# Performance work log

Hardware: AMD Instinct MI355X
Metric: run time of the kernel (lower is better)

Reference implementation:

```python
import jax, jax.numpy as jnp
import numpy as np

EPS = 1e-12  # torch F.normalize eps


def _l2norm(x):
    n = jnp.sqrt(jnp.sum(x * x, axis=-1, keepdims=True))
    return x / jnp.maximum(n, EPS)


def setup_inputs() -> dict:
    key = jax.random.key(0)
    k1, k2, k3, k4 = jax.random.split(key, 4)
    Bq, Lq, Bd, Ld, H, D = 128, 32, 128, 128, 256, 128
    return {
        "query_h": jax.random.normal(k1, (Bq, Lq, H), dtype=jnp.float32),
        "doc_h": jax.random.normal(k2, (Bd, Ld, H), dtype=jnp.float32),
        "W": jax.random.normal(k3, (H, D), dtype=jnp.float32) * 0.02,
        "b": jax.random.normal(k4, (D,), dtype=jnp.float32) * 0.02,
    }


def reference(query_h, doc_h, W, b):
    # token_mapper + L2 normalize (as in embed())
    q = _l2norm(query_h @ W + b)          # [Bq, Lq, D]
    d = _l2norm(doc_h @ W + b)            # [Bd, Ld, D]
    # max_sim: cross-product bmm(doc, query^T) -> [Bq, Bd, Ld, Lq]
    scores = jnp.einsum('qsd,btd->qbts', q, d)
    # max over doc tokens (dim=1 of bmm output), sum over query tokens (dim=2)
    logits = jnp.sum(jnp.max(scores, axis=2), axis=2)  # [Bq, Bd]
    return logits
```

## Files before the change

kernel.cpp:

```cpp
#include <hip/hip_runtime.h>

typedef unsigned short u16;
typedef __attribute__((ext_vector_type(8))) short short8;
typedef __attribute__((ext_vector_type(16))) float f32x16;
typedef __attribute__((ext_vector_type(4))) float f32x4;
typedef __attribute__((ext_vector_type(2))) float f32x2;
typedef __attribute__((ext_vector_type(4))) unsigned int u32x4;

#define H 256
#define D 128


static __device__ inline u16 f32_to_bf16(float f) {
    unsigned u = __float_as_uint(f);
    unsigned r = u + 0x7FFFu + ((u >> 16) & 1u);
    return (u16)(r >> 16);
}

__global__ __launch_bounds__(256) void proj_norm_fused(
    const float* __restrict__ Xq, const float* __restrict__ Xd,
    const float* __restrict__ W,  const float* __restrict__ bias,
    u16* __restrict__ outq, u16* __restrict__ outd)
{
    __shared__ float xs[64][33];
    __shared__ float ws[64][128];
    const int blk = blockIdx.x;
    const float* X;
    u16* out;
    int tok0;
    if (blk < 128) { X = Xq; out = outq; tok0 = blk * 32; }
    else           { X = Xd; out = outd; tok0 = (blk - 128) * 32; }

    const int tid = threadIdx.x;
    const int tg = tid >> 5;
    const int dg = tid & 31;

    float acc[4][4] = {{0.f}};

    for (int h0 = 0; h0 < H; h0 += 64) {
        {
            int c  = tid & 15;
            int tp = tid >> 4;
            #pragma unroll
            for (int pass = 0; pass < 2; ++pass) {
                int t = tp + pass * 16;
                f32x4 v = *(const f32x4*)&X[(size_t)(tok0 + t) * H + h0 + c * 4];
                xs[c*4+0][t] = v.x;
                xs[c*4+1][t] = v.y;
                xs[c*4+2][t] = v.z;
                xs[c*4+3][t] = v.w;
            }
        }
        {
            int dcol = tid & 31;
            int hrow = tid >> 5;
            #pragma unroll
            for (int pass = 0; pass < 8; ++pass) {
                int hh = hrow + pass * 8;
                *(f32x4*)&ws[hh][dcol*4] =
                    *(const f32x4*)&W[(size_t)(h0 + hh) * D + dcol * 4];
            }
        }
        __syncthreads();
        #pragma unroll 8
        for (int hh = 0; hh < 64; ++hh) {
            float x0 = xs[hh][tg*4+0];
            float x1 = xs[hh][tg*4+1];
            float x2 = xs[hh][tg*4+2];
            float x3 = xs[hh][tg*4+3];
            f32x4 wv = *(const f32x4*)&ws[hh][dg*4];
            #pragma unroll
            for (int j = 0; j < 4; ++j) {
                acc[0][j] += x0 * wv[j];
                acc[1][j] += x1 * wv[j];
                acc[2][j] += x2 * wv[j];
                acc[3][j] += x3 * wv[j];
            }
        }
        __syncthreads();
    }

    f32x4 bv = *(const f32x4*)&bias[dg * 4];
    #pragma unroll
    for (int i = 0; i < 4; ++i)
        #pragma unroll
        for (int j = 0; j < 4; ++j)
            acc[i][j] += bv[j];

    const int kc   = dg >> 2;
    const int lg2  = (dg >> 1) & 1;
    const int par  = dg & 1;
    const size_t tileBase = (size_t)(tok0 >> 5) * 4096;

    #pragma unroll
    for (int i = 0; i < 4; ++i) {
        float ss = acc[i][0]*acc[i][0] + acc[i][1]*acc[i][1]
                 + acc[i][2]*acc[i][2] + acc[i][3]*acc[i][3];
        ss += __shfl_xor(ss, 1);
        ss += __shfl_xor(ss, 2);
        ss += __shfl_xor(ss, 4);
        ss += __shfl_xor(ss, 8);
        ss += __shfl_xor(ss, 16);
        float n   = sqrtf(ss);
        float inv = 1.0f / fmaxf(n, 1e-12f);
        unsigned p0 = (unsigned)f32_to_bf16(acc[i][0]*inv) |
                      ((unsigned)f32_to_bf16(acc[i][1]*inv) << 16);
        unsigned p1 = (unsigned)f32_to_bf16(acc[i][2]*inv) |
                      ((unsigned)f32_to_bf16(acc[i][3]*inv) << 16);
        unsigned q0 = __shfl_xor(p0, 1);
        unsigned q1 = __shfl_xor(p1, 1);
        if ((par == 0) == (i < 2)) {
            u32x4 ck;
            if (par == 0) { ck.x = p0; ck.y = p1; ck.z = q0; ck.w = q1; }
            else          { ck.x = q0; ck.y = q1; ck.z = p0; ck.w = p1; }
            int l31 = tg * 4 + i;
            *(u32x4*)&out[tileBase + kc * 512 + l31 * 16 + lg2 * 8] = ck;
        }
    }
}

__global__ __launch_bounds__(256) void maxsim_kernel(
    const u16* __restrict__ qbf, const u16* __restrict__ dbf,
    float* __restrict__ logits)
{
    __shared__ float smax[4][8][2][32];
    const int tid  = threadIdx.x;
    const int wid  = tid >> 6;
    const int lane = tid & 63;
    const int l31  = lane & 31;
    const int soff = ((lane & 31) * 2 + (lane >> 5)) * 8;

    const int qb0 = (blockIdx.x >> 4) * 2;
    const int db0 = (blockIdx.x & 15) * 8;

    short8 bq[2][8];
    #pragma unroll
    for (int qs = 0; qs < 2; ++qs) {
        const u16* qb_base = qbf + (size_t)(qb0 + qs) * 4096 + soff;
        #pragma unroll
        for (int kc = 0; kc < 8; ++kc)
            bq[qs][kc] = *(const short8*)(qb_base + kc * 512);
    }

    #pragma unroll 2
    for (int dbi = 0; dbi < 8; ++dbi) {
        const u16* dt = dbf + (size_t)((db0 + dbi) * 4 + wid) * 4096 + soff;
        short8 af[8];
        #pragma unroll
        for (int kc = 0; kc < 8; ++kc)
            af[kc] = *(const short8*)(dt + kc * 512);

        f32x16 acc0 = {0.f}, acc1 = {0.f};
        #pragma unroll
        for (int kc = 0; kc < 8; ++kc) {
            acc0 = __builtin_amdgcn_mfma_f32_32x32x16_bf16(af[kc], bq[0][kc], acc0, 0, 0, 0);
            acc1 = __builtin_amdgcn_mfma_f32_32x32x16_bf16(af[kc], bq[1][kc], acc1, 0, 0, 0);
        }

        #pragma unroll
        for (int qs = 0; qs < 2; ++qs) {
            const f32x16 a = qs ? acc1 : acc0;
            float m0 = fmaxf(a[0], a[1]),   m1 = fmaxf(a[2], a[3]);
            float m2 = fmaxf(a[4], a[5]),   m3 = fmaxf(a[6], a[7]);
            float m4 = fmaxf(a[8], a[9]),   m5 = fmaxf(a[10], a[11]);
            float m6 = fmaxf(a[12], a[13]), m7 = fmaxf(a[14], a[15]);
            float m = fmaxf(fmaxf(fmaxf(m0, m1), fmaxf(m2, m3)),
                            fmaxf(fmaxf(m4, m5), fmaxf(m6, m7)));
            m = fmaxf(m, __shfl_xor(m, 32));
            if (lane < 32) smax[wid][dbi][qs][l31] = m;
        }
    }
    __syncthreads();

    {
        const int dbi = tid >> 5;
        const int col = tid & 31;
        float v0 = fmaxf(fmaxf(smax[0][dbi][0][col], smax[1][dbi][0][col]),
                         fmaxf(smax[2][dbi][0][col], smax[3][dbi][0][col]));
        float v1 = fmaxf(fmaxf(smax[0][dbi][1][col], smax[1][dbi][1][col]),
                         fmaxf(smax[2][dbi][1][col], smax[3][dbi][1][col]));
        v0 += __shfl_xor(v0, 1);  v1 += __shfl_xor(v1, 1);
        v0 += __shfl_xor(v0, 2);  v1 += __shfl_xor(v1, 2);
        v0 += __shfl_xor(v0, 4);  v1 += __shfl_xor(v1, 4);
        v0 += __shfl_xor(v0, 8);  v1 += __shfl_xor(v1, 8);
        v0 += __shfl_xor(v0, 16); v1 += __shfl_xor(v1, 16);
        if (col == 0) {
            logits[(size_t)qb0 * 128 + db0 + dbi]       = v0;
            logits[(size_t)(qb0 + 1) * 128 + db0 + dbi] = v1;
        }
    }
}

extern "C" void kernel_launch(void* const* d_in, const int* in_sizes, int n_in,
                              void* d_out, int out_size, void* d_ws, size_t ws_size,
                              hipStream_t stream)
{
    const float* query_h = (const float*)d_in[0];
    const float* doc_h   = (const float*)d_in[1];
    const float* W       = (const float*)d_in[2];
    const float* bias    = (const float*)d_in[3];
    float* logits = (float*)d_out;

    u16* qbf = (u16*)d_ws;
    u16* dbf = qbf + (size_t)128 * 4096;

    proj_norm_fused<<<dim3(640), dim3(256), 0, stream>>>(query_h, doc_h, W, bias, qbf, dbf);
    maxsim_kernel<<<dim3(1024), dim3(256), 0, stream>>>(qbf, dbf, logits);
}
```

Measured before the change: 114.5 us.

## Replace FP32 FMA projection with split-bf16 MFMA projection and W pre-pack

The scalar FP32 shared-memory GEMM for the token projection is replaced by MFMA 32x32x16 bf16 instructions. Each operand is split into a high bf16 part and a low residual, and three MFMAs per tile approximate FP32 accuracy. A new small prep kernel packs W into hi/lo bf16 fragments laid out for the MFMA. Normalization and the tiled bf16 output layout are recomputed from the MFMA accumulator layout. This adds a kernel launch and leaves only 160 blocks, which may underfill the GPU.

```diff
diff --git a/kernel.cpp b/kernel.cpp
--- a/kernel.cpp
+++ b/kernel.cpp
@@ -1,120 +1,149 @@
 #include <hip/hip_runtime.h>
 
 typedef unsigned short u16;
+typedef unsigned int u32;
 typedef __attribute__((ext_vector_type(8))) short short8;
 typedef __attribute__((ext_vector_type(16))) float f32x16;
 typedef __attribute__((ext_vector_type(4))) float f32x4;
-typedef __attribute__((ext_vector_type(2))) float f32x2;
 typedef __attribute__((ext_vector_type(4))) unsigned int u32x4;
 
 #define H 256
 #define D 128
 
 
-static __device__ inline u16 f32_to_bf16(float f) {
-    unsigned u = __float_as_uint(f);
-    unsigned r = u + 0x7FFFu + ((u >> 16) & 1u);
-    return (u16)(r >> 16);
-}
-
-__global__ __launch_bounds__(256) void proj_norm_fused(
+union V16 { u32x4 u; short8 s; f32x4 f; };
+
+static __device__ inline u32 bf16pk_rne(float a, float b) {
+    u32 ua = __float_as_uint(a), ub = __float_as_uint(b);
+    ua = ua + 0x7FFFu + ((ua >> 16) & 1u);
+    ub = ub + 0x7FFFu + ((ub >> 16) & 1u);
+    return (ua >> 16) | (ub & 0xFFFF0000u);
+}
+
+__global__ __launch_bounds__(256) void prep_w(
+    const float* __restrict__ W, u16* __restrict__ whi, u16* __restrict__ wlo)
+{
+    const int g   = blockIdx.x * 256 + threadIdx.x;
+    const int slot = g & 63;
+    const int kc  = (g >> 6) & 15;
+    const int nt  = g >> 10;
+    const int l31 = slot >> 1;
+    const int lg2 = slot & 1;
+    const int k0  = kc * 16 + lg2 * 8;
+    const int n   = nt * 32 + l31;
+
+    u32 hw[4], lw[4];
+    #pragma unroll
+    for (int p = 0; p < 4; ++p) {
+        float a = W[(size_t)(k0 + 2*p)     * D + n];
+        float b = W[(size_t)(k0 + 2*p + 1) * D + n];
+        u32 ua = __float_as_uint(a), ub = __float_as_uint(b);
+        u32 ha = ua & 0xFFFF0000u,   hb = ub & 0xFFFF0000u;
+        hw[p] = (ua >> 16) | hb;
+        float la = a - __uint_as_float(ha);
+        float lb = b - __uint_as_float(hb);
+        u32 ra = __float_as_uint(la); ra += 0x7FFFu + ((ra >> 16) & 1u);
+        u32 rb = __float_as_uint(lb); rb += 0x7FFFu + ((rb >> 16) & 1u);
+        lw[p] = (ra >> 16) | (rb & 0xFFFF0000u);
+    }
+    u32x4 hv = {hw[0], hw[1], hw[2], hw[3]};
+    u32x4 lv = {lw[0], lw[1], lw[2], lw[3]};
+    *(u32x4*)&whi[(size_t)g * 8] = hv;
+    *(u32x4*)&wlo[(size_t)g * 8] = lv;
+}
+
+__global__ __launch_bounds__(256) void proj_mfma(
     const float* __restrict__ Xq, const float* __restrict__ Xd,
-    const float* __restrict__ W,  const float* __restrict__ bias,
+    const float* __restrict__ bias,
+    const u16* __restrict__ whi, const u16* __restrict__ wlo,
     u16* __restrict__ outq, u16* __restrict__ outd)
 {
-    __shared__ float xs[64][33];
-    __shared__ float ws[64][128];
-    const int blk = blockIdx.x;
-    const float* X;
-    u16* out;
-    int tok0;
-    if (blk < 128) { X = Xq; out = outq; tok0 = blk * 32; }
-    else           { X = Xd; out = outd; tok0 = (blk - 128) * 32; }
-
-    const int tid = threadIdx.x;
-    const int tg = tid >> 5;
-    const int dg = tid & 31;
-
-    float acc[4][4] = {{0.f}};
-
-    for (int h0 = 0; h0 < H; h0 += 64) {
-        {
-            int c  = tid & 15;
-            int tp = tid >> 4;
+    const int tid  = threadIdx.x;
+    const int wid  = tid >> 6;
+    const int lane = tid & 63;
+    const int l31  = lane & 31;
+    const int hi   = lane >> 5;
+    const int slot = l31 * 2 + hi;
+
+    const float* X; u16* out; int trow0;
+    if (blockIdx.x < 32) { X = Xq; out = outq; trow0 = blockIdx.x * 128 + wid * 32; }
+    else { X = Xd; out = outd; trow0 = (blockIdx.x - 32) * 128 + wid * 32; }
+
+    const float* xrow = X + (size_t)(trow0 + l31) * H + hi * 8;
+
+    f32x16 acc[4];
+    #pragma unroll
+    for (int nt = 0; nt < 4; ++nt) acc[nt] = (f32x16){0.f};
+
+    #pragma unroll
+    for (int kc = 0; kc < 16; ++kc) {
+        V16 a4, b4;
+        a4.f = *(const f32x4*)(xrow + kc * 16);
+        b4.f = *(const f32x4*)(xrow + kc * 16 + 4);
+        float e[8];
+        #pragma unroll
+        for (int i = 0; i < 4; ++i) { e[i] = a4.f[i]; e[i + 4] = b4.f[i]; }
+
+        V16 xh, xl;
+        u32 xhu[4], xlu[4];
+        #pragma unroll
+        for (int p = 0; p < 4; ++p) {
+            u32 u0 = __float_as_uint(e[2*p]), u1 = __float_as_uint(e[2*p+1]);
+            u32 h0 = u0 & 0xFFFF0000u,        h1 = u1 & 0xFFFF0000u;
+            xhu[p] = (u0 >> 16) | h1;
+            float l0 = e[2*p]   - __uint_as_float(h0);
+            float l1 = e[2*p+1] - __uint_as_float(h1);
+            xlu[p] = (__float_as_uint(l0) >> 16) |
+                     (__float_as_uint(l1) & 0xFFFF0000u);
+        }
+        xh.u = (u32x4){xhu[0], xhu[1], xhu[2], xhu[3]};
+        xl.u = (u32x4){xlu[0], xlu[1], xlu[2], xlu[3]};
+
+        #pragma unroll
+        for (int nt = 0; nt < 4; ++nt) {
+            V16 wh, wl;
+            const size_t fo = (size_t)((nt * 16 + kc) * 64 + slot) * 8;
+            wh.u = *(const u32x4*)&whi[fo];
+            wl.u = *(const u32x4*)&wlo[fo];
+            acc[nt] = __builtin_amdgcn_mfma_f32_32x32x16_bf16(wh.s, xh.s, acc[nt], 0, 0, 0);
+            acc[nt] = __builtin_amdgcn_mfma_f32_32x32x16_bf16(wl.s, xh.s, acc[nt], 0, 0, 0);
+            acc[nt] = __builtin_amdgcn_mfma_f32_32x32x16_bf16(wh.s, xl.s, acc[nt], 0, 0, 0);
+        }
+    }
+
+    float ss = 0.f;
+    #pragma unroll
+    for (int nt = 0; nt < 4; ++nt) {
+        #pragma unroll
+        for (int q = 0; q < 4; ++q) {
+            f32x4 b4 = *(const f32x4*)&bias[nt * 32 + q * 8 + hi * 4];
             #pragma unroll
-            for (int pass = 0; pass < 2; ++pass) {
-                int t = tp + pass * 16;
-                f32x4 v = *(const f32x4*)&X[(size_t)(tok0 + t) * H + h0 + c * 4];
-                xs[c*4+0][t] = v.x;
-                xs[c*4+1][t] = v.y;
-                xs[c*4+2][t] = v.z;
-                xs[c*4+3][t] = v.w;
+            for (int i = 0; i < 4; ++i) {
+                float v = acc[nt][q*4+i] + b4[i];
+                acc[nt][q*4+i] = v;
+                ss += v * v;
             }
         }
-        {
-            int dcol = tid & 31;
-            int hrow = tid >> 5;
-            #pragma unroll
-            for (int pass = 0; pass < 8; ++pass) {
-                int hh = hrow + pass * 8;
-                *(f32x4*)&ws[hh][dcol*4] =
-                    *(const f32x4*)&W[(size_t)(h0 + hh) * D + dcol * 4];
+    }
+    ss += __shfl_xor(ss, 32);
+    const float inv = 1.0f / fmaxf(sqrtf(ss), 1e-12f);
+
+    const size_t base = (size_t)(trow0 >> 5) * 4096;
+    #pragma unroll
+    for (int nt = 0; nt < 4; ++nt) {
+        #pragma unroll
+        for (int q = 0; q < 4; ++q) {
+            float v0 = acc[nt][q*4+0] * inv, v1 = acc[nt][q*4+1] * inv;
+            float v2 = acc[nt][q*4+2] * inv, v3 = acc[nt][q*4+3] * inv;
+            u32 p0 = bf16pk_rne(v0, v1), p1 = bf16pk_rne(v2, v3);
+            u32 r0 = __shfl_xor(p0, 32), r1 = __shfl_xor(p1, 32);
+            if ((q & 1) == hi) {
+                const int kc = nt * 2 + (q >> 1);
+                u32x4 ck;
+                if (hi == 0) ck = (u32x4){p0, p1, r0, r1};
+                else         ck = (u32x4){r0, r1, p0, p1};
+                *(u32x4*)&out[base + (size_t)kc * 512 + (size_t)slot * 8] = ck;
             }
-        }
-        __syncthreads();
-        #pragma unroll 8
-        for (int hh = 0; hh < 64; ++hh) {
-            float x0 = xs[hh][tg*4+0];
-            float x1 = xs[hh][tg*4+1];
-            float x2 = xs[hh][tg*4+2];
-            float x3 = xs[hh][tg*4+3];
-            f32x4 wv = *(const f32x4*)&ws[hh][dg*4];
-            #pragma unroll
-            for (int j = 0; j < 4; ++j) {
-                acc[0][j] += x0 * wv[j];
-                acc[1][j] += x1 * wv[j];
-                acc[2][j] += x2 * wv[j];
-                acc[3][j] += x3 * wv[j];
-            }
-        }
-        __syncthreads();
-    }
-
-    f32x4 bv = *(const f32x4*)&bias[dg * 4];
-    #pragma unroll
-    for (int i = 0; i < 4; ++i)
-        #pragma unroll
-        for (int j = 0; j < 4; ++j)
-            acc[i][j] += bv[j];
-
-    const int kc   = dg >> 2;
-    const int lg2  = (dg >> 1) & 1;
-    const int par  = dg & 1;
-    const size_t tileBase = (size_t)(tok0 >> 5) * 4096;
-
-    #pragma unroll
-    for (int i = 0; i < 4; ++i) {
-        float ss = acc[i][0]*acc[i][0] + acc[i][1]*acc[i][1]
-                 + acc[i][2]*acc[i][2] + acc[i][3]*acc[i][3];
-        ss += __shfl_xor(ss, 1);
-        ss += __shfl_xor(ss, 2);
-        ss += __shfl_xor(ss, 4);
-        ss += __shfl_xor(ss, 8);
-        ss += __shfl_xor(ss, 16);
-        float n   = sqrtf(ss);
-        float inv = 1.0f / fmaxf(n, 1e-12f);
-        unsigned p0 = (unsigned)f32_to_bf16(acc[i][0]*inv) |
-                      ((unsigned)f32_to_bf16(acc[i][1]*inv) << 16);
-        unsigned p1 = (unsigned)f32_to_bf16(acc[i][2]*inv) |
-                      ((unsigned)f32_to_bf16(acc[i][3]*inv) << 16);
-        unsigned q0 = __shfl_xor(p0, 1);
-        unsigned q1 = __shfl_xor(p1, 1);
-        if ((par == 0) == (i < 2)) {
-            u32x4 ck;
-            if (par == 0) { ck.x = p0; ck.y = p1; ck.z = q0; ck.w = q1; }
-            else          { ck.x = q0; ck.y = q1; ck.z = p0; ck.w = p1; }
-            int l31 = tg * 4 + i;
-            *(u32x4*)&out[tileBase + kc * 512 + l31 * 16 + lg2 * 8] = ck;
         }
     }
 }
@@ -203,7 +232,10 @@
 
     u16* qbf = (u16*)d_ws;
     u16* dbf = qbf + (size_t)128 * 4096;
-
-    proj_norm_fused<<<dim3(640), dim3(256), 0, stream>>>(query_h, doc_h, W, bias, qbf, dbf);
+    u16* whi = dbf + (size_t)512 * 4096;
+    u16* wlo = whi + (size_t)4096 * 8;
+
+    prep_w   <<<dim3(16),   dim3(256), 0, stream>>>(W, whi, wlo);
+    proj_mfma<<<dim3(160),  dim3(256), 0, stream>>>(query_h, doc_h, bias, whi, wlo, qbf, dbf);
     maxsim_kernel<<<dim3(1024), dim3(256), 0, stream>>>(qbf, dbf, logits);
 }
```

New measurement: 105.5 us. 7.9% less time.
